# Performance work log

Hardware: AMD Instinct MI355X
Metric: run time of the kernel (lower is better)

Reference implementation:

```python
import jax, jax.numpy as jnp
import numpy as np

B, S, NK, H, D, DM = 2, 2048, 32, 8, 64, 512
NEG = -1e9


def setup_inputs() -> dict:
    key = jax.random.key(0)
    ks = jax.random.split(key, 12)
    hidden_states = jax.random.normal(ks[0], (B, S, DM), jnp.float32)
    rpe = jax.random.normal(ks[1], (B, S, NK, H), jnp.float32)
    idx = jax.random.randint(ks[2], (S, NK), 0, S)
    pad = jax.random.uniform(ks[3], (S, NK)) < 0.1
    q_k_mask = jnp.where(pad, -1, idx).astype(jnp.int32)
    k_q_mask = jax.random.randint(ks[4], (S, NK), 0, S).astype(jnp.int32)  # only used by TVM backward
    sc = 0.02
    w_q = jax.random.normal(ks[5], (DM, H * D), jnp.float32) * sc
    w_k = jax.random.normal(ks[6], (DM, H * D), jnp.float32) * sc
    w_v = jax.random.normal(ks[7], (DM, H * D), jnp.float32) * sc
    fc_w = jax.random.normal(ks[8], (H * D, DM), jnp.float32) * sc
    fc_b = jnp.zeros((DM,), jnp.float32)
    ln_g = jnp.ones((DM,), jnp.float32)
    ln_b = jnp.zeros((DM,), jnp.float32)
    return {"hidden_states": hidden_states, "rpe": rpe, "q_k_mask": q_k_mask,
            "k_q_mask": k_q_mask, "w_q": w_q, "w_k": w_k, "w_v": w_v,
            "fc_w": fc_w, "fc_b": fc_b, "ln_g": ln_g, "ln_b": ln_b}


def reference(hidden_states, rpe, q_k_mask, k_q_mask, w_q, w_k, w_v, fc_w, fc_b, ln_g, ln_b):
    bsz, seq_len, _ = hidden_states.shape
    q = (hidden_states @ w_q).reshape(bsz, seq_len, H, D)
    k = (hidden_states @ w_k).reshape(bsz, seq_len, H, D)
    v = (hidden_states @ w_v).reshape(bsz, seq_len, H, D)

    valid = q_k_mask >= 0                      # [S, NK]
    idx = jnp.where(valid, q_k_mask, 0)        # safe gather index
    vmask = valid[None, :, None, :]            # [1,S,1,NK] broadcast over (b, h)

    # QKP_mm_tvm: sparse QK^T over neighbor lists, plus relative-position bias,
    # padded slots -> -1e9.  k_g: [B,S,NK,H,D]
    k_g = k[:, idx]
    scores = jnp.einsum('bshd,bsnhd->bshn', q, k_g) + rpe.transpose(0, 1, 3, 2)
    scores = jnp.where(vmask, scores, NEG)
    scores = scores / (D ** 0.5)

    attn = jax.nn.softmax(scores, axis=-1)
    # AttnV_mm_tvm with padding 0: padded slots contribute nothing.
    attn = attn * vmask
    v_g = v[:, idx]                            # [B,S,NK,H,D]
    ctx = jnp.einsum('bshn,bsnhd->bshd', attn, v_g).reshape(bsz, seq_len, H * D)

    out = ctx @ fc_w + fc_b + hidden_states    # dropout = identity (eval)
    mu = jnp.mean(out, axis=-1, keepdims=True)
    var = jnp.mean((out - mu) ** 2, axis=-1, keepdims=True)
    return (out - mu) * jax.lax.rsqrt(var + 1e-6) * ln_g + ln_b
```

## Files before the change

kernel.cpp:

```cpp
#include <hip/hip_runtime.h>
#include <hip/hip_bf16.h>

constexpr int Bb  = 2;
constexpr int Ss  = 2048;
constexpr int NKk = 32;
constexpr int Hh  = 8;
constexpr int DMm = 512;
constexpr int Mm  = Bb * Ss;
constexpr int QKV = 1536;

typedef __attribute__((ext_vector_type(8))) short bf16x8;
typedef __attribute__((ext_vector_type(4))) float f32x4;

__device__ __forceinline__ float b2f(unsigned short u) {
  return __uint_as_float((unsigned)u << 16);
}
__device__ __forceinline__ unsigned short f2b(float f) {
  unsigned u = __float_as_uint(f);
  unsigned r = (u + 0x7fffu + ((u >> 16) & 1u)) >> 16;
  return (unsigned short)r;
}
__device__ __forceinline__ void gload_lds16(const ushort* g, ushort* l) {
  __builtin_amdgcn_global_load_lds(
      (const __attribute__((address_space(1))) void*)g,
      (__attribute__((address_space(3))) void*)l, 16, 0, 0);
}

__global__ __launch_bounds__(256) void cvt_all_k(
    const float* __restrict__ hs,
    const float* __restrict__ Wq, const float* __restrict__ Wk,
    const float* __restrict__ Wv, const float* __restrict__ Wf,
    ushort* __restrict__ Xb, ushort* __restrict__ Wt3, ushort* __restrict__ Wtf)
{
  __shared__ float tile[64][65];
  const int z = blockIdx.z;
  const int t = threadIdx.x;

  if (z >= 4) {
    const int cid = (z - 4) * 64 + blockIdx.x * 8 + blockIdx.y;
    const size_t base8 = (size_t)cid * 1024;
#pragma unroll
    for (int it = 0; it < 4; ++it) {
      const size_t i = base8 + it * 256 + t;
      const float4 a = reinterpret_cast<const float4*>(hs)[2 * i];
      const float4 b = reinterpret_cast<const float4*>(hs)[2 * i + 1];
      ushort o[8] = {f2b(a.x), f2b(a.y), f2b(a.z), f2b(a.w),
                     f2b(b.x), f2b(b.y), f2b(b.z), f2b(b.w)};
      reinterpret_cast<uint4*>(Xb)[i] = *reinterpret_cast<uint4*>(o);
    }
    return;
  }

  const float* W = (z == 0) ? Wq : (z == 1) ? Wk : (z == 2) ? Wv : Wf;
  ushort* Wt = (z < 3) ? (Wt3 + (size_t)z * 512 * 512) : Wtf;

  const int k0 = blockIdx.x * 64, n0 = blockIdx.y * 64;
#pragma unroll
  for (int p = 0; p < 4; ++p) {
    const int r = (t >> 4) + p * 16, c = (t & 15) * 4;
    const float4 v = *reinterpret_cast<const float4*>(&W[(size_t)(k0 + r) * 512 + n0 + c]);
    tile[r][c] = v.x; tile[r][c + 1] = v.y; tile[r][c + 2] = v.z; tile[r][c + 3] = v.w;
  }
  __syncthreads();
  const int n = t >> 2, ks = (t & 3) * 16;
  ushort o[16];
#pragma unroll
  for (int i = 0; i < 16; ++i) o[i] = f2b(tile[ks + i][n]);
  *reinterpret_cast<uint4*>(&Wt[(size_t)(n0 + n) * 512 + k0 + ks])     = *reinterpret_cast<uint4*>(&o[0]);
  *reinterpret_cast<uint4*>(&Wt[(size_t)(n0 + n) * 512 + k0 + ks + 8]) = *reinterpret_cast<uint4*>(&o[8]);
}

template <int OUT_BF16, int BMv, int BNv>
__global__ __launch_bounds__(256) void gemm_dbuf(
    const ushort* __restrict__ Xb, const ushort* __restrict__ Wt,
    void* __restrict__ Yv, const float* __restrict__ bias,
    const float* __restrict__ resid, int ldY)
{
  constexpr int MI = BMv / 32;
  constexpr int NJ = BNv / 32;
  constexpr int ASZ = BMv * 64;
  __shared__ ushort smem[2 * ASZ + 2 * BNv * 64];

  const int bm = blockIdx.x * BMv;
  const int bn = blockIdx.y * BNv;
  const int t  = threadIdx.x;
  const int wave = t >> 6, lane = t & 63;
  const int wm = (wave >> 1) * (BMv / 2);
  const int wn = (wave & 1) * (BNv / 2);

  f32x4 acc[MI][NJ] = {};

  auto stage = [&](int buf, int k0) {
    ushort* A = smem + buf * ASZ;
    ushort* B = smem + 2 * ASZ + buf * (BNv * 64);
#pragma unroll
    for (int p = 0; p < MI; ++p) {
      const int i = p * 256 + t;
      const int row = i >> 3, sb = i & 7;
      gload_lds16(Xb + (size_t)(bm + row) * 512 + k0 + ((sb ^ (row & 7)) << 3),
                  &A[(size_t)(p * 256 + wave * 64) * 8]);
    }
#pragma unroll
    for (int p = 0; p < NJ; ++p) {
      const int i = p * 256 + t;
      const int row = i >> 3, sb = i & 7;
      gload_lds16(Wt + (size_t)(bn + row) * 512 + k0 + ((sb ^ (row & 7)) << 3),
                  &B[(size_t)(p * 256 + wave * 64) * 8]);
    }
  };

  auto compute = [&](int buf) {
    const ushort* A = smem + buf * ASZ;
    const ushort* B = smem + 2 * ASZ + buf * (BNv * 64);
#pragma unroll
    for (int ks = 0; ks < 2; ++ks) {
      const int kb = ks * 4 + (lane >> 4);
      bf16x8 af[MI], bfr[NJ];
#pragma unroll
      for (int i = 0; i < MI; ++i) {
        const int row = wm + i * 16 + (lane & 15);
        af[i] = *reinterpret_cast<const bf16x8*>(&A[row * 64 + ((kb ^ (row & 7)) << 3)]);
      }
#pragma unroll
      for (int j = 0; j < NJ; ++j) {
        const int row = wn + j * 16 + (lane & 15);
        bfr[j] = *reinterpret_cast<const bf16x8*>(&B[row * 64 + ((kb ^ (row & 7)) << 3)]);
      }
#pragma unroll
      for (int i = 0; i < MI; ++i)
#pragma unroll
        for (int j = 0; j < NJ; ++j)
          acc[i][j] = __builtin_amdgcn_mfma_f32_16x16x32_bf16(af[i], bfr[j], acc[i][j], 0, 0, 0);
    }
  };

  stage(0, 0);
  __syncthreads();
  int cur = 0;
  for (int k0 = 64; k0 < 512; k0 += 64) {
    stage(cur ^ 1, k0);
    compute(cur);
    __syncthreads();
    cur ^= 1;
  }
  compute(cur);

  if (OUT_BF16) {
    __syncthreads();
#pragma unroll
    for (int i = 0; i < MI; ++i)
#pragma unroll
      for (int j = 0; j < NJ; ++j)
#pragma unroll
        for (int r = 0; r < 4; ++r) {
          const int row = wm + i * 16 + (lane >> 4) * 4 + r;
          const int col = wn + j * 16 + (lane & 15);
          smem[row * BNv + col] = f2b(acc[i][j][r]);
        }
    __syncthreads();
    ushort* Y = reinterpret_cast<ushort*>(Yv);
    constexpr int CPT = BMv * BNv / 8 / 256;
#pragma unroll
    for (int p = 0; p < CPT; ++p) {
      const int c = p * 256 + t;
      const int row = c / (BNv / 8);
      const int cb  = c % (BNv / 8);
      *reinterpret_cast<uint4*>(&Y[(size_t)(bm + row) * ldY + bn + cb * 8]) =
          *reinterpret_cast<uint4*>(&smem[row * BNv + cb * 8]);
    }
  } else {
    float* Y = reinterpret_cast<float*>(Yv);
#pragma unroll
    for (int i = 0; i < MI; ++i) {
#pragma unroll
      for (int j = 0; j < NJ; ++j) {
        const int m = bm + wm + i * 16 + (lane >> 4) * 4;
        const int n = bn + wn + j * 16 + (lane & 15);
        const float bb = bias[n];
#pragma unroll
        for (int r = 0; r < 4; ++r)
          Y[(size_t)(m + r) * ldY + n] = acc[i][j][r] + bb + resid[(size_t)(m + r) * 512 + n];
      }
    }
  }
}

__global__ __launch_bounds__(256) void attn_k5(
    const ushort* __restrict__ qkv, const float* __restrict__ rpe,
    const int* __restrict__ qkm, ushort* __restrict__ ctx)
{
  __shared__ ushort Ks[32 * 512];
  __shared__ float  qs[512];

  const int bs = blockIdx.x;
  const int b  = bs >> 11;
  const int s  = bs & 2047;
  const int t  = threadIdx.x;
  const int wv = t >> 6, lane = t & 63;

  const uint qu = *reinterpret_cast<const uint*>(qkv + (size_t)bs * QKV + 2 * t);
  qs[2 * t]     = __uint_as_float(qu << 16);
  qs[2 * t + 1] = __uint_as_float(qu & 0xffff0000u);

  const int iv = qkm[s * NKk + (lane & 31)];
  const float rv = rpe[((size_t)bs * NKk + (t & 31)) * Hh + (t >> 5)];

#pragma unroll
  for (int r = 0; r < 8; ++r) {
    const int n = r * 4 + wv;
    int im = qkm[s * NKk + n];
    im = im < 0 ? 0 : im;
    const ushort* gsrc = qkv + (size_t)(b * Ss + im) * QKV + 512
                       + ((lane ^ (n & 7)) * 8);
    gload_lds16(gsrc, &Ks[n * 512]);
  }

  const ushort* vbase = qkv + (size_t)b * Ss * QKV + 1024;
  const int e = 2 * t;
  uint vvu[32];
#pragma unroll
  for (int n2 = 0; n2 < 32; ++n2) {
    int row = __shfl(iv, (lane & 32) + n2, 64);
    row = row < 0 ? 0 : row;
    vvu[n2] = *reinterpret_cast<const uint*>(&vbase[(size_t)row * QKV + (e & 511)]);
  }

  __syncthreads();

  const int h = t >> 5;
  const int n = t & 31;
  const bool valid = (iv >= 0);

  float2 a2 = make_float2(0.f, 0.f);
#pragma unroll
  for (int j = 0; j < 8; ++j) {
    const int blk = (h * 8 + j) ^ (n & 7);
    const uint4 kk = *reinterpret_cast<const uint4*>(&Ks[n * 512 + blk * 8]);
    const float4 qa = *reinterpret_cast<const float4*>(&qs[h * 64 + j * 8]);
    const float4 qb = *reinterpret_cast<const float4*>(&qs[h * 64 + j * 8 + 4]);
    a2.x += qa.x * __uint_as_float(kk.x << 16);
    a2.y += qa.y * __uint_as_float(kk.x & 0xffff0000u);
    a2.x += qa.z * __uint_as_float(kk.y << 16);
    a2.y += qa.w * __uint_as_float(kk.y & 0xffff0000u);
    a2.x += qb.x * __uint_as_float(kk.z << 16);
    a2.y += qb.y * __uint_as_float(kk.z & 0xffff0000u);
    a2.x += qb.z * __uint_as_float(kk.w << 16);
    a2.y += qb.w * __uint_as_float(kk.w & 0xffff0000u);
  }
  float sc = a2.x + a2.y + rv;
  sc = valid ? sc * 0.125f : -1e30f;

  float mx = sc;
#pragma unroll
  for (int m = 16; m >= 1; m >>= 1) mx = fmaxf(mx, __shfl_xor(mx, m, 32));
  const float p = valid ? __expf(sc - mx) : 0.f;
  float sum = p;
#pragma unroll
  for (int m = 16; m >= 1; m >>= 1) sum += __shfl_xor(sum, m, 32);
  const float pn = (sum > 0.f) ? (p / sum) : 0.f;

  float c0 = 0.f, c1 = 0.f;
#pragma unroll
  for (int n2 = 0; n2 < 32; ++n2) {
    const float a = __shfl(pn, (lane & 32) + n2, 64);
    c0 += a * __uint_as_float(vvu[n2] << 16);
    c1 += a * __uint_as_float(vvu[n2] & 0xffff0000u);
  }
  const uint packed = (uint)f2b(c0) | ((uint)f2b(c1) << 16);
  *reinterpret_cast<uint*>(&ctx[(size_t)bs * 512 + e]) = packed;
}

__global__ __launch_bounds__(256) void ln_k(
    float* __restrict__ x, const float* __restrict__ g,
    const float* __restrict__ bta)
{
  const int w    = threadIdx.x >> 6;
  const int lane = threadIdx.x & 63;
  const int row  = blockIdx.x * 4 + w;

  float4* xr = reinterpret_cast<float4*>(x + (size_t)row * 512);
  const float4 v0 = xr[lane];
  const float4 v1 = xr[lane + 64];

  float sum = v0.x + v0.y + v0.z + v0.w + v1.x + v1.y + v1.z + v1.w;
  float sq  = v0.x * v0.x + v0.y * v0.y + v0.z * v0.z + v0.w * v0.w
            + v1.x * v1.x + v1.y * v1.y + v1.z * v1.z + v1.w * v1.w;
#pragma unroll
  for (int m = 32; m >= 1; m >>= 1) {
    sum += __shfl_xor(sum, m, 64);
    sq  += __shfl_xor(sq,  m, 64);
  }
  const float mu  = sum * (1.f / 512.f);
  const float var = sq * (1.f / 512.f) - mu * mu;
  const float rs  = rsqrtf(var + 1e-6f);

  const float4 g0 = reinterpret_cast<const float4*>(g)[lane];
  const float4 g1 = reinterpret_cast<const float4*>(g)[lane + 64];
  const float4 b0 = reinterpret_cast<const float4*>(bta)[lane];
  const float4 b1 = reinterpret_cast<const float4*>(bta)[lane + 64];

  float4 o0, o1;
  o0.x = (v0.x - mu) * rs * g0.x + b0.x;
  o0.y = (v0.y - mu) * rs * g0.y + b0.y;
  o0.z = (v0.z - mu) * rs * g0.z + b0.z;
  o0.w = (v0.w - mu) * rs * g0.w + b0.w;
  o1.x = (v1.x - mu) * rs * g1.x + b1.x;
  o1.y = (v1.y - mu) * rs * g1.y + b1.y;
  o1.z = (v1.z - mu) * rs * g1.z + b1.z;
  o1.w = (v1.w - mu) * rs * g1.w + b1.w;
  xr[lane]      = o0;
  xr[lane + 64] = o1;
}

extern "C" void kernel_launch(void* const* d_in, const int* in_sizes, int n_in,
                              void* d_out, int out_size, void* d_ws, size_t ws_size,
                              hipStream_t stream) {
  const float* hs  = (const float*)d_in[0];
  const float* rpe = (const float*)d_in[1];
  const int*   qkm = (const int*)d_in[2];
  const float* wq  = (const float*)d_in[4];
  const float* wk  = (const float*)d_in[5];
  const float* wv  = (const float*)d_in[6];
  const float* fcw = (const float*)d_in[7];
  const float* fcb = (const float*)d_in[8];
  const float* lng = (const float*)d_in[9];
  const float* lnb = (const float*)d_in[10];
  float* out = (float*)d_out;

  ushort* Xb  = (ushort*)d_ws;
  ushort* Wt3 = Xb  + (size_t)Mm * DMm;
  ushort* Wtf = Wt3 + (size_t)3 * DMm * DMm;
  ushort* qkv = Wtf + (size_t)DMm * DMm;
  ushort* cxb = qkv + (size_t)Mm * QKV;

  cvt_all_k<<<dim3(8, 8, 8), 256, 0, stream>>>(hs, wq, wk, wv, fcw, Xb, Wt3, Wtf);

  gemm_dbuf<1, 128, 96><<<dim3(Mm / 128, QKV / 96), 256, 0, stream>>>(
      Xb, Wt3, qkv, nullptr, nullptr, QKV);

  attn_k5<<<Mm, 256, 0, stream>>>(qkv, rpe, qkm, cxb);

  gemm_dbuf<0, 128, 64><<<dim3(Mm / 128, DMm / 64), 256, 0, stream>>>(
      cxb, Wtf, out, fcb, hs, DMm);
  ln_k<<<Mm / 4, 256, 0, stream>>>(out, lng, lnb);
}
```

Before: 57.15 us.

## Fuse LayerNorm into output GEMM via last-block counter and pipeline GEMM loads

Removes the separate LayerNorm launch. Each output-GEMM block increments a per-row-tile atomic counter, and the last block to finish a 128-row stripe normalizes those rows in place. The GEMM main loop now uses explicit vmcnt waits and raw s_barriers, so the next stage's loads stay in flight while the current tile computes. The attention kernel loads q differently and moves its barrier ahead of the V gathers. This adds a memset launch and serializes the LayerNorm tail onto one block per stripe, which could lengthen the kernel's tail.

New measurement: 94.39 us. 65.2% more time.

```diff
diff --git a/kernel.cpp b/kernel.cpp
--- a/kernel.cpp
+++ b/kernel.cpp
@@ -71,15 +71,19 @@
 }
 
 template <int OUT_BF16, int BMv, int BNv>
-__global__ __launch_bounds__(256) void gemm_dbuf(
+__global__ __launch_bounds__(256) void gemm_pipe(
     const ushort* __restrict__ Xb, const ushort* __restrict__ Wt,
     void* __restrict__ Yv, const float* __restrict__ bias,
-    const float* __restrict__ resid, int ldY)
+    const float* __restrict__ resid, int ldY,
+    const float* __restrict__ lng, const float* __restrict__ lnb,
+    int* __restrict__ cnt)
 {
-  constexpr int MI = BMv / 32;
-  constexpr int NJ = BNv / 32;
+  constexpr int MI  = BMv / 32;
+  constexpr int NJ  = BNv / 32;
+  constexpr int STG = MI + NJ;
   constexpr int ASZ = BMv * 64;
   __shared__ ushort smem[2 * ASZ + 2 * BNv * 64];
+  __shared__ int lastflag;
 
   const int bm = blockIdx.x * BMv;
   const int bn = blockIdx.y * BNv;
@@ -135,18 +139,24 @@
   };
 
   stage(0, 0);
-  __syncthreads();
   int cur = 0;
-  for (int k0 = 64; k0 < 512; k0 += 64) {
-    stage(cur ^ 1, k0);
+#pragma unroll
+  for (int i = 0; i < 8; ++i) {
+    if (i < 7) {
+      stage(cur ^ 1, (i + 1) * 64);
+      asm volatile("s_waitcnt vmcnt(%0)" :: "n"(STG) : "memory");
+    } else {
+      asm volatile("s_waitcnt vmcnt(0)" ::: "memory");
+    }
+    __builtin_amdgcn_sched_barrier(0);
+    __builtin_amdgcn_s_barrier();
     compute(cur);
-    __syncthreads();
+    __builtin_amdgcn_sched_barrier(0);
+    __builtin_amdgcn_s_barrier();
     cur ^= 1;
   }
-  compute(cur);
 
   if (OUT_BF16) {
-    __syncthreads();
 #pragma unroll
     for (int i = 0; i < MI; ++i)
 #pragma unroll
@@ -182,10 +192,51 @@
           Y[(size_t)(m + r) * ldY + n] = acc[i][j][r] + bb + resid[(size_t)(m + r) * 512 + n];
       }
     }
-  }
-}
-
-__global__ __launch_bounds__(256) void attn_k5(
+
+    __threadfence();
+    if (t == 0) lastflag = atomicAdd(&cnt[blockIdx.x], 1);
+    __syncthreads();
+    if (lastflag == (int)gridDim.y - 1) {
+      __threadfence();
+      const int w = t >> 6, ln = t & 63;
+#pragma unroll 4
+      for (int p = 0; p < BMv / 4; ++p) {
+        const int row = bm + p * 4 + w;
+        float4* xr = reinterpret_cast<float4*>(Y + (size_t)row * 512);
+        const float4 v0 = xr[ln];
+        const float4 v1 = xr[ln + 64];
+        float sum = v0.x + v0.y + v0.z + v0.w + v1.x + v1.y + v1.z + v1.w;
+        float sq  = v0.x * v0.x + v0.y * v0.y + v0.z * v0.z + v0.w * v0.w
+                  + v1.x * v1.x + v1.y * v1.y + v1.z * v1.z + v1.w * v1.w;
+#pragma unroll
+        for (int m = 32; m >= 1; m >>= 1) {
+          sum += __shfl_xor(sum, m, 64);
+          sq  += __shfl_xor(sq,  m, 64);
+        }
+        const float mu  = sum * (1.f / 512.f);
+        const float var = sq * (1.f / 512.f) - mu * mu;
+        const float rs  = rsqrtf(var + 1e-6f);
+        const float4 g0 = reinterpret_cast<const float4*>(lng)[ln];
+        const float4 g1 = reinterpret_cast<const float4*>(lng)[ln + 64];
+        const float4 b0 = reinterpret_cast<const float4*>(lnb)[ln];
+        const float4 b1 = reinterpret_cast<const float4*>(lnb)[ln + 64];
+        float4 o0, o1;
+        o0.x = (v0.x - mu) * rs * g0.x + b0.x;
+        o0.y = (v0.y - mu) * rs * g0.y + b0.y;
+        o0.z = (v0.z - mu) * rs * g0.z + b0.z;
+        o0.w = (v0.w - mu) * rs * g0.w + b0.w;
+        o1.x = (v1.x - mu) * rs * g1.x + b1.x;
+        o1.y = (v1.y - mu) * rs * g1.y + b1.y;
+        o1.z = (v1.z - mu) * rs * g1.z + b1.z;
+        o1.w = (v1.w - mu) * rs * g1.w + b1.w;
+        xr[ln]      = o0;
+        xr[ln + 64] = o1;
+      }
+    }
+  }
+}
+
+__global__ __launch_bounds__(256) void attn_k6(
     const ushort* __restrict__ qkv, const float* __restrict__ rpe,
     const int* __restrict__ qkm, ushort* __restrict__ ctx)
 {
@@ -198,12 +249,9 @@
   const int t  = threadIdx.x;
   const int wv = t >> 6, lane = t & 63;
 
-  const uint qu = *reinterpret_cast<const uint*>(qkv + (size_t)bs * QKV + 2 * t);
-  qs[2 * t]     = __uint_as_float(qu << 16);
-  qs[2 * t + 1] = __uint_as_float(qu & 0xffff0000u);
-
-  const int iv = qkm[s * NKk + (lane & 31)];
-  const float rv = rpe[((size_t)bs * NKk + (t & 31)) * Hh + (t >> 5)];
+  const ushort* qrow = qkv + (size_t)bs * QKV;
+  qs[t]       = b2f(qrow[t]);
+  qs[t + 256] = b2f(qrow[t + 256]);
 
 #pragma unroll
   for (int r = 0; r < 8; ++r) {
@@ -215,6 +263,11 @@
     gload_lds16(gsrc, &Ks[n * 512]);
   }
 
+  const int iv = qkm[s * NKk + (lane & 31)];
+  const float rv = rpe[((size_t)bs * NKk + (t & 31)) * Hh + (t >> 5)];
+
+  __syncthreads();
+
   const ushort* vbase = qkv + (size_t)b * Ss * QKV + 1024;
   const int e = 2 * t;
   uint vvu[32];
@@ -224,8 +277,6 @@
     row = row < 0 ? 0 : row;
     vvu[n2] = *reinterpret_cast<const uint*>(&vbase[(size_t)row * QKV + (e & 511)]);
   }
-
-  __syncthreads();
 
   const int h = t >> 5;
   const int n = t & 31;
@@ -268,48 +319,6 @@
   }
   const uint packed = (uint)f2b(c0) | ((uint)f2b(c1) << 16);
   *reinterpret_cast<uint*>(&ctx[(size_t)bs * 512 + e]) = packed;
-}
-
-__global__ __launch_bounds__(256) void ln_k(
-    float* __restrict__ x, const float* __restrict__ g,
-    const float* __restrict__ bta)
-{
-  const int w    = threadIdx.x >> 6;
-  const int lane = threadIdx.x & 63;
-  const int row  = blockIdx.x * 4 + w;
-
-  float4* xr = reinterpret_cast<float4*>(x + (size_t)row * 512);
-  const float4 v0 = xr[lane];
-  const float4 v1 = xr[lane + 64];
-
-  float sum = v0.x + v0.y + v0.z + v0.w + v1.x + v1.y + v1.z + v1.w;
-  float sq  = v0.x * v0.x + v0.y * v0.y + v0.z * v0.z + v0.w * v0.w
-            + v1.x * v1.x + v1.y * v1.y + v1.z * v1.z + v1.w * v1.w;
-#pragma unroll
-  for (int m = 32; m >= 1; m >>= 1) {
-    sum += __shfl_xor(sum, m, 64);
-    sq  += __shfl_xor(sq,  m, 64);
-  }
-  const float mu  = sum * (1.f / 512.f);
-  const float var = sq * (1.f / 512.f) - mu * mu;
-  const float rs  = rsqrtf(var + 1e-6f);
-
-  const float4 g0 = reinterpret_cast<const float4*>(g)[lane];
-  const float4 g1 = reinterpret_cast<const float4*>(g)[lane + 64];
-  const float4 b0 = reinterpret_cast<const float4*>(bta)[lane];
-  const float4 b1 = reinterpret_cast<const float4*>(bta)[lane + 64];
-
-  float4 o0, o1;
-  o0.x = (v0.x - mu) * rs * g0.x + b0.x;
-  o0.y = (v0.y - mu) * rs * g0.y + b0.y;
-  o0.z = (v0.z - mu) * rs * g0.z + b0.z;
-  o0.w = (v0.w - mu) * rs * g0.w + b0.w;
-  o1.x = (v1.x - mu) * rs * g1.x + b1.x;
-  o1.y = (v1.y - mu) * rs * g1.y + b1.y;
-  o1.z = (v1.z - mu) * rs * g1.z + b1.z;
-  o1.w = (v1.w - mu) * rs * g1.w + b1.w;
-  xr[lane]      = o0;
-  xr[lane + 64] = o1;
 }
 
 extern "C" void kernel_launch(void* const* d_in, const int* in_sizes, int n_in,
@@ -332,15 +341,17 @@
   ushort* Wtf = Wt3 + (size_t)3 * DMm * DMm;
   ushort* qkv = Wtf + (size_t)DMm * DMm;
   ushort* cxb = qkv + (size_t)Mm * QKV;
+  int*    cnt = (int*)(cxb + (size_t)Mm * DMm);
+
+  hipMemsetAsync(cnt, 0, 32 * sizeof(int), stream);
 
   cvt_all_k<<<dim3(8, 8, 8), 256, 0, stream>>>(hs, wq, wk, wv, fcw, Xb, Wt3, Wtf);
 
-  gemm_dbuf<1, 128, 96><<<dim3(Mm / 128, QKV / 96), 256, 0, stream>>>(
-      Xb, Wt3, qkv, nullptr, nullptr, QKV);
-
-  attn_k5<<<Mm, 256, 0, stream>>>(qkv, rpe, qkm, cxb);
-
-  gemm_dbuf<0, 128, 64><<<dim3(Mm / 128, DMm / 64), 256, 0, stream>>>(
-      cxb, Wtf, out, fcb, hs, DMm);
-  ln_k<<<Mm / 4, 256, 0, stream>>>(out, lng, lnb);
-}
+  gemm_pipe<1, 128, 96><<<dim3(Mm / 128, QKV / 96), 256, 0, stream>>>(
+      Xb, Wt3, qkv, nullptr, nullptr, QKV, nullptr, nullptr, nullptr);
+
+  attn_k6<<<Mm, 256, 0, stream>>>(qkv, rpe, qkm, cxb);
+
+  gemm_pipe<0, 128, 64><<<dim3(Mm / 128, DMm / 64), 256, 0, stream>>>(
+      cxb, Wtf, out, fcb, hs, DMm, lng, lnb, cnt);
+}
```

## Pipeline GEMM K-loop with explicit vmcnt waits and reorder attention loads

Applied to the files above, without the earlier changes.

The GEMM main loop is fully unrolled and uses explicit s_waitcnt vmcnt plus raw s_barrier with sched_barriers. The next tile's async global-to-LDS loads can then stay in flight while the current tile is computed, instead of draining at every __syncthreads. In the attention kernel, the q load is split into scalar bf16 reads, the index and rpe loads move after the K gather issue, and the barrier moves before the V gathers, so V loads overlap with the QK dot product. The hand-counted vmcnt depends on the number of loads per stage matching STG, which is fragile if the compiler emits a different number of loads.

Result: faster. 55.38 us (-3.1%).

```diff
diff --git a/kernel.cpp b/kernel.cpp
--- a/kernel.cpp
+++ b/kernel.cpp
@@ -71,13 +71,14 @@
 }
 
 template <int OUT_BF16, int BMv, int BNv>
-__global__ __launch_bounds__(256) void gemm_dbuf(
+__global__ __launch_bounds__(256) void gemm_pipe(
     const ushort* __restrict__ Xb, const ushort* __restrict__ Wt,
     void* __restrict__ Yv, const float* __restrict__ bias,
     const float* __restrict__ resid, int ldY)
 {
-  constexpr int MI = BMv / 32;
-  constexpr int NJ = BNv / 32;
+  constexpr int MI  = BMv / 32;
+  constexpr int NJ  = BNv / 32;
+  constexpr int STG = MI + NJ;
   constexpr int ASZ = BMv * 64;
   __shared__ ushort smem[2 * ASZ + 2 * BNv * 64];
 
@@ -135,18 +136,24 @@
   };
 
   stage(0, 0);
-  __syncthreads();
   int cur = 0;
-  for (int k0 = 64; k0 < 512; k0 += 64) {
-    stage(cur ^ 1, k0);
+#pragma unroll
+  for (int i = 0; i < 8; ++i) {
+    if (i < 7) {
+      stage(cur ^ 1, (i + 1) * 64);
+      asm volatile("s_waitcnt vmcnt(%0)" :: "n"(STG) : "memory");
+    } else {
+      asm volatile("s_waitcnt vmcnt(0)" ::: "memory");
+    }
+    __builtin_amdgcn_sched_barrier(0);
+    __builtin_amdgcn_s_barrier();
     compute(cur);
-    __syncthreads();
+    __builtin_amdgcn_sched_barrier(0);
+    __builtin_amdgcn_s_barrier();
     cur ^= 1;
   }
-  compute(cur);
 
   if (OUT_BF16) {
-    __syncthreads();
 #pragma unroll
     for (int i = 0; i < MI; ++i)
 #pragma unroll
@@ -185,7 +192,7 @@
   }
 }
 
-__global__ __launch_bounds__(256) void attn_k5(
+__global__ __launch_bounds__(256) void attn_k6(
     const ushort* __restrict__ qkv, const float* __restrict__ rpe,
     const int* __restrict__ qkm, ushort* __restrict__ ctx)
 {
@@ -198,12 +205,9 @@
   const int t  = threadIdx.x;
   const int wv = t >> 6, lane = t & 63;
 
-  const uint qu = *reinterpret_cast<const uint*>(qkv + (size_t)bs * QKV + 2 * t);
-  qs[2 * t]     = __uint_as_float(qu << 16);
-  qs[2 * t + 1] = __uint_as_float(qu & 0xffff0000u);
-
-  const int iv = qkm[s * NKk + (lane & 31)];
-  const float rv = rpe[((size_t)bs * NKk + (t & 31)) * Hh + (t >> 5)];
+  const ushort* qrow = qkv + (size_t)bs * QKV;
+  qs[t]       = b2f(qrow[t]);
+  qs[t + 256] = b2f(qrow[t + 256]);
 
 #pragma unroll
   for (int r = 0; r < 8; ++r) {
@@ -215,6 +219,11 @@
     gload_lds16(gsrc, &Ks[n * 512]);
   }
 
+  const int iv = qkm[s * NKk + (lane & 31)];
+  const float rv = rpe[((size_t)bs * NKk + (t & 31)) * Hh + (t >> 5)];
+
+  __syncthreads();
+
   const ushort* vbase = qkv + (size_t)b * Ss * QKV + 1024;
   const int e = 2 * t;
   uint vvu[32];
@@ -224,8 +233,6 @@
     row = row < 0 ? 0 : row;
     vvu[n2] = *reinterpret_cast<const uint*>(&vbase[(size_t)row * QKV + (e & 511)]);
   }
-
-  __syncthreads();
 
   const int h = t >> 5;
   const int n = t & 31;
@@ -335,12 +342,12 @@
 
   cvt_all_k<<<dim3(8, 8, 8), 256, 0, stream>>>(hs, wq, wk, wv, fcw, Xb, Wt3, Wtf);
 
-  gemm_dbuf<1, 128, 96><<<dim3(Mm / 128, QKV / 96), 256, 0, stream>>>(
+  gemm_pipe<1, 128, 96><<<dim3(Mm / 128, QKV / 96), 256, 0, stream>>>(
       Xb, Wt3, qkv, nullptr, nullptr, QKV);
 
-  attn_k5<<<Mm, 256, 0, stream>>>(qkv, rpe, qkm, cxb);
-
-  gemm_dbuf<0, 128, 64><<<dim3(Mm / 128, DMm / 64), 256, 0, stream>>>(
+  attn_k6<<<Mm, 256, 0, stream>>>(qkv, rpe, qkm, cxb);
+
+  gemm_pipe<0, 128, 64><<<dim3(Mm / 128, DMm / 64), 256, 0, stream>>>(
       cxb, Wtf, out, fcb, hs, DMm);
   ln_k<<<Mm / 4, 256, 0, stream>>>(out, lng, lnb);
 }
```
